# Performance work log

Hardware: AMD Instinct MI355X
Metric: run time of the kernel (lower is better)

## Reference

```python
import jax, jax.numpy as jnp
import numpy as np

B, T, D = 2, 1024, 2048      # batch, seq, model dim
E, F, K = 64, 512, 4          # n_experts, expert hidden, top-k
S, HS = 2, 512 * 4            # shared experts, shared hidden = expert_dim * topk


def setup_inputs() -> dict:
    key = jax.random.key(0)
    ks = jax.random.split(key, 9)
    s = 0.02
    f32 = jnp.float32
    return {
        "x": jax.random.normal(ks[0], (B, T, D), f32),
        "router_w": jax.random.normal(ks[1], (D, E), f32) * s,
        "router_bias": jnp.zeros((E,), f32),
        "wg": jax.random.normal(ks[2], (E, D, F), f32) * s,
        "wu": jax.random.normal(ks[3], (E, D, F), f32) * s,
        "wd": jax.random.normal(ks[4], (E, F, D), f32) * s,
        "swg": jax.random.normal(ks[5], (S, D, HS), f32) * s,
        "swu": jax.random.normal(ks[6], (S, D, HS), f32) * s,
        "swd": jax.random.normal(ks[7], (S, HS, D), f32) * s,
    }


def reference(x, router_w, router_bias, wg, wu, wd, swg, swu, swd):
    b, t, d = x.shape
    flat = x.reshape(b * t, d)                      # [N, D]
    n = flat.shape[0]

    # Router: softmax scores, top-k selection on (logits + bias)
    logits = flat @ router_w                         # [N, E]
    scores = jax.nn.softmax(logits, axis=-1)
    _, topk_idx = jax.lax.top_k(logits + router_bias, K)          # [N, K]
    topk_scores = jnp.take_along_axis(scores, topk_idx, axis=-1)  # [N, K]
    topk_scores = topk_scores / topk_scores.sum(axis=-1, keepdims=True)

    # Dense combine weights: w[n, e] = normalized score if expert e selected else 0
    comb = jnp.zeros((n, E), dtype=flat.dtype).at[
        jnp.arange(n)[:, None], topk_idx].set(topk_scores)        # [N, E]

    # Routed experts (SwiGLU), computed densely and masked by combine weights
    g = jax.nn.silu(jnp.einsum('nd,edf->nef', flat, wg))          # [N, E, F]
    u = jnp.einsum('nd,edf->nef', flat, wu)                       # [N, E, F]
    routed = jnp.einsum('ne,nef,efd->nd', comb, g * u, wd)        # [N, D]

    # Shared experts (always active, summed)
    sg = jax.nn.silu(jnp.einsum('nd,sdh->nsh', flat, swg))        # [N, S, HS]
    su = jnp.einsum('nd,sdh->nsh', flat, swu)
    shared = jnp.einsum('nsh,shd->nd', sg * su, swd)              # [N, D]

    return (routed + shared).reshape(b, t, d)
```

## Files before the change

### kernel.cpp

```cpp
#include <hip/hip_runtime.h>
#include <hip/hip_bf16.h>

typedef __bf16 bf16x8 __attribute__((ext_vector_type(8)));
typedef float f32x4 __attribute__((ext_vector_type(4)));
typedef unsigned short u16x4 __attribute__((ext_vector_type(4)));
typedef unsigned short u16x8 __attribute__((ext_vector_type(8)));

#define DEVI __device__ __forceinline__

constexpr int N_TOK = 2048;
constexpr int DIM   = 2048;
constexpr int NEXP  = 64;
constexpr int FDIM  = 512;
constexpr int TOPK  = 4;
constexpr int NSH   = 2;
constexpr int HSH   = 2048;

#define WAIT_VM0 asm volatile("s_waitcnt vmcnt(0)" ::: "memory")
#define WAIT_VM3 asm volatile("s_waitcnt vmcnt(3)" ::: "memory")
#define WAIT_VM4 asm volatile("s_waitcnt vmcnt(4)" ::: "memory")
#define WAIT_VM6 asm volatile("s_waitcnt vmcnt(6)" ::: "memory")
#define WAIT_LG0 asm volatile("s_waitcnt lgkmcnt(0)" ::: "memory")
#define SBAR __builtin_amdgcn_s_barrier()

DEVI unsigned short f2b(float f) {
  union { float fv; unsigned u; } v; v.fv = f;
  unsigned r = v.u + 0x7fffu + ((v.u >> 16) & 1u);
  return (unsigned short)(r >> 16);
}
DEVI float b2f(unsigned short h) {
  union { unsigned u; float f; } v; v.u = ((unsigned)h) << 16;
  return v.f;
}
DEVI void gll16(const void* g, void* l) {
  __builtin_amdgcn_global_load_lds((const __attribute__((address_space(1))) unsigned*)g,
                                   (__attribute__((address_space(3))) unsigned*)l, 16, 0, 0);
}
DEVI unsigned cvtpk(float lo, float hi) {
  unsigned r;
  asm("v_cvt_pk_bf16_f32 %0, %1, %2" : "=v"(r) : "v"(lo), "v"(hi));
  return r;
}
DEVI bf16x8 fragB(const float* base, int str) {
  union { unsigned u[4]; bf16x8 v; } r;
  #pragma unroll
  for (int p = 0; p < 4; ++p) r.u[p] = cvtpk(base[(2 * p) * str], base[(2 * p + 1) * str]);
  return r.v;
}

__global__ void cvt_x_kernel(const float* __restrict__ x, unsigned short* __restrict__ xb) {
  const size_t i = ((size_t)blockIdx.x * 256 + threadIdx.x) * 8;
  const float4 a = *reinterpret_cast<const float4*>(x + i);
  const float4 b = *reinterpret_cast<const float4*>(x + i + 4);
  u16x8 o;
  o[0] = f2b(a.x); o[1] = f2b(a.y); o[2] = f2b(a.z); o[3] = f2b(a.w);
  o[4] = f2b(b.x); o[5] = f2b(b.y); o[6] = f2b(b.z); o[7] = f2b(b.w);
  *reinterpret_cast<u16x8*>(xb + i) = o;
}

__global__ __launch_bounds__(256)
void tr_shared_kernel(const float* __restrict__ swu, const float* __restrict__ swg,
                      const float* __restrict__ swd, unsigned short* __restrict__ swuT,
                      unsigned short* __restrict__ swgT, unsigned short* __restrict__ swdT) {
  __shared__ float Lf[64][68];
  const int tid = threadIdx.x;
  const int r0 = blockIdx.x * 64, c0 = blockIdx.y * 64;
  const int z = blockIdx.z, mat = z >> 1;
  const size_t soff = (size_t)(z & 1) * DIM * HSH;
  const float* in = (mat == 0 ? swu : mat == 1 ? swg : swd) + soff;
  unsigned short* ot = (mat == 0 ? swuT : mat == 1 ? swgT : swdT) + soff;
  #pragma unroll
  for (int j = 0; j < 4; ++j) {
    const int idx = j * 1024 + tid * 4;
    const int row = idx >> 6, col = idx & 63;
    const float4 v = *reinterpret_cast<const float4*>(in + (size_t)(r0 + row) * 2048 + c0 + col);
    *reinterpret_cast<float4*>(&Lf[row][col]) = v;
  }
  __syncthreads();
  #pragma unroll
  for (int j = 0; j < 4; ++j) {
    const int idx = j * 1024 + tid * 4;
    const int orow = idx >> 6, ocol = idx & 63;
    u16x4 o;
    o[0] = f2b(Lf[ocol][orow]);     o[1] = f2b(Lf[ocol + 1][orow]);
    o[2] = f2b(Lf[ocol + 2][orow]); o[3] = f2b(Lf[ocol + 3][orow]);
    *reinterpret_cast<u16x4*>(ot + (size_t)(c0 + orow) * 2048 + r0 + ocol) = o;
  }
}

__global__ __launch_bounds__(256)
void router_kernel(const float* __restrict__ x, const float* __restrict__ rw,
                   const float* __restrict__ rb, int* __restrict__ cnt,
                   int* __restrict__ listTok, float* __restrict__ listW,
                   int* __restrict__ tokEP) {
  __shared__ float Lx[8][128];
  const int tid = threadIdx.x;
  const int lane = tid & 63;
  const int wave = tid >> 6;
  const int tokBase = blockIdx.x * 8;

  float acc0 = 0.f, acc1 = 0.f;
  for (int dc = 0; dc < DIM; dc += 128) {
    __syncthreads();
    {
      const int idx = tid * 4;
      const int row = idx >> 7, col = idx & 127;
      *reinterpret_cast<float4*>(&Lx[row][col]) =
          *reinterpret_cast<const float4*>(x + (size_t)(tokBase + row) * DIM + dc + col);
    }
    __syncthreads();
    #pragma unroll 16
    for (int dd = 0; dd < 128; ++dd) {
      const float r = rw[(size_t)(dc + dd) * NEXP + lane];
      acc0 = fmaf(Lx[wave * 2 + 0][dd], r, acc0);
      acc1 = fmaf(Lx[wave * 2 + 1][dd], r, acc1);
    }
  }

  const float bias = rb[lane];
  #pragma unroll
  for (int t = 0; t < 2; ++t) {
    const float v = (t == 0) ? acc0 : acc1;
    const int token = tokBase + wave * 2 + t;
    float m = v;
    #pragma unroll
    for (int o = 32; o > 0; o >>= 1) m = fmaxf(m, __shfl_xor(m, o));
    const float p = expf(v - m);
    float ss = p;
    #pragma unroll
    for (int o = 32; o > 0; o >>= 1) ss += __shfl_xor(ss, o);
    const float score = p / ss;
    float cur = v + bias;
    float wk[TOPK]; int ik[TOPK]; float wsum = 0.f;
    #pragma unroll
    for (int k = 0; k < TOPK; ++k) {
      float tm = cur;
      #pragma unroll
      for (int o = 32; o > 0; o >>= 1) tm = fmaxf(tm, __shfl_xor(tm, o));
      const unsigned long long msk = __ballot(cur == tm);
      const int sel = (int)__builtin_ctzll(msk);
      const float w = __shfl(score, sel);
      wk[k] = w; ik[k] = sel; wsum += w;
      if (lane == sel) cur = -3.4e38f;
    }
    if (lane < TOPK) {
      const int e = ik[lane];
      const float w = wk[lane] / wsum;
      const int slot = atomicAdd(&cnt[e], 1);
      listTok[(size_t)e * N_TOK + slot] = token;
      listW[(size_t)e * N_TOK + slot] = w;
      tokEP[token * TOPK + lane] = (e << 16) | slot;
    }
  }
}

__global__ void scan_kernel(const int* __restrict__ cnt, int* __restrict__ off) {
  if (threadIdx.x == 0) {
    int s = 0;
    for (int e = 0; e < NEXP; ++e) { off[e] = s; s += cnt[e]; }
  }
}

__global__ __launch_bounds__(256, 3)
void up_routed(const unsigned short* __restrict__ xb,
               const float* __restrict__ Wu, const float* __restrict__ Wg,
               const int* __restrict__ cnt, const int* __restrict__ off,
               const int* __restrict__ listTok, const float* __restrict__ listW,
               unsigned short* __restrict__ H) {
  constexpr int NT = DIM / 32;
  const int tid = threadIdx.x;
  const int f0 = blockIdx.x * 64;
  const int e  = blockIdx.y;
  const int m0 = blockIdx.z * 128;
  const int c = cnt[e];
  if (m0 >= c) return;
  const int rcnt = min(128, c - m0);
  const int rowbase = off[e] + m0;

  __shared__ __align__(16) unsigned short Al[2][4][128][8];
  __shared__ __align__(16) float Bf[2][2][32][64];
  __shared__ float wSs[128];

  if (tid < 128) wSs[tid] = (tid < rcnt) ? listW[(size_t)e * N_TOK + m0 + tid] : 0.f;
  WAIT_LG0;

  const int wid = tid >> 6, l = tid & 63;
  const int wm = wid >> 1, wn = wid & 1;
  const int lc = l & 15, hi = l >> 4;

  const int t0 = listTok[(size_t)e * N_TOK + m0 + min(l, rcnt - 1)];
  const int t1 = listTok[(size_t)e * N_TOK + m0 + min(64 + l, rcnt - 1)];
  const unsigned short* pa0 = xb + (size_t)t0 * DIM;
  const unsigned short* pa1 = xb + (size_t)t1 * DIM;
  const unsigned short* pas = (wid & 1) ? pa1 : pa0;
  const float* pbu = Wu + (size_t)e * DIM * FDIM + (size_t)(l >> 4) * FDIM + f0 + (l & 15) * 4;
  const float* pbg = Wg + (size_t)e * DIM * FDIM + (size_t)(l >> 4) * FDIM + f0 + (l & 15) * 4;

  auto stage = [&](int g, int b) {
    const int d0 = g * 32;
    gll16(pas + d0 + (wid >> 1) * 8,      &Al[b][wid >> 1][(wid & 1) * 64][0]);
    gll16(pas + d0 + (wid >> 1) * 8 + 16, &Al[b][(wid >> 1) + 2][(wid & 1) * 64][0]);
    gll16(pbu + (size_t)(d0 + 4 * wid) * FDIM,      &Bf[b][0][4 * wid][0]);
    gll16(pbu + (size_t)(d0 + 4 * wid + 16) * FDIM, &Bf[b][0][4 * wid + 16][0]);
    gll16(pbg + (size_t)(d0 + 4 * wid) * FDIM,      &Bf[b][1][4 * wid][0]);
    gll16(pbg + (size_t)(d0 + 4 * wid + 16) * FDIM, &Bf[b][1][4 * wid + 16][0]);
  };

  f32x4 aU[4][2], aG[4][2];
  #pragma unroll
  for (int i = 0; i < 4; ++i)
    #pragma unroll
    for (int j = 0; j < 2; ++j) { aU[i][j] = f32x4{0,0,0,0}; aG[i][j] = f32x4{0,0,0,0}; }

  stage(0, 0);
  for (int g = 0; g < NT; ++g) {
    const int b = g & 1;
    if (g + 1 < NT) { stage(g + 1, b ^ 1); WAIT_VM6; } else { WAIT_VM0; }
    SBAR;
    bf16x8 af[4];
    #pragma unroll
    for (int mi = 0; mi < 4; ++mi)
      af[mi] = *reinterpret_cast<const bf16x8*>(&Al[b][hi][wm * 64 + mi * 16 + lc][0]);
    #pragma unroll
    for (int ni = 0; ni < 2; ++ni) {
      const bf16x8 bu = fragB(&Bf[b][0][hi * 8][wn * 32 + ni * 16 + lc], 64);
      const bf16x8 bg = fragB(&Bf[b][1][hi * 8][wn * 32 + ni * 16 + lc], 64);
      #pragma unroll
      for (int mi = 0; mi < 4; ++mi) {
        aU[mi][ni] = __builtin_amdgcn_mfma_f32_16x16x32_bf16(af[mi], bu, aU[mi][ni], 0, 0, 0);
        aG[mi][ni] = __builtin_amdgcn_mfma_f32_16x16x32_bf16(af[mi], bg, aG[mi][ni], 0, 0, 0);
      }
    }
    SBAR;
  }

  #pragma unroll
  for (int mi = 0; mi < 4; ++mi)
    #pragma unroll
    for (int ni = 0; ni < 2; ++ni)
      #pragma unroll
      for (int r2 = 0; r2 < 4; ++r2) {
        const int row = wm * 64 + mi * 16 + hi * 4 + r2;
        if (row < rcnt) {
          const int col = f0 + wn * 32 + ni * 16 + lc;
          const float g = aG[mi][ni][r2], u = aU[mi][ni][r2];
          const float h = (g / (1.f + __expf(-g))) * u * wSs[row];
          H[(size_t)(rowbase + row) * FDIM + col] = f2b(h);
        }
      }
}

__global__ __launch_bounds__(256, 3)
void down_routed(const unsigned short* __restrict__ Hr, const float* __restrict__ wd,
                 const int* __restrict__ cnt, const int* __restrict__ off,
                 unsigned short* __restrict__ P) {
  constexpr int NT = FDIM / 32;
  const int tid = threadIdx.x;
  const int x0 = blockIdx.x * 128;
  const int e  = blockIdx.y;
  const int m0 = blockIdx.z * 128;
  const int c = cnt[e];
  if (m0 >= c) return;
  const int rcnt = min(128, c - m0);
  const int rowbase = off[e] + m0;

  __shared__ __align__(16) unsigned short Al[2][4][128][8];
  __shared__ __align__(16) float Bf[2][32][128];

  const int wid = tid >> 6, l = tid & 63;
  const int wm = wid >> 1, wn = wid & 1;
  const int lc = l & 15, hi = l >> 4;

  const unsigned short* pa0 = Hr + (size_t)(rowbase + min(l, rcnt - 1)) * FDIM;
  const unsigned short* pa1 = Hr + (size_t)(rowbase + min(64 + l, rcnt - 1)) * FDIM;
  const unsigned short* pas = (wid & 1) ? pa1 : pa0;
  const float* pB = wd + (size_t)e * FDIM * DIM + (size_t)(l >> 5) * DIM + x0 + (l & 31) * 4;

  auto stage = [&](int g, int b) {
    const int d0 = g * 32;
    gll16(pas + d0 + (wid >> 1) * 8,      &Al[b][wid >> 1][(wid & 1) * 64][0]);
    gll16(pas + d0 + (wid >> 1) * 8 + 16, &Al[b][(wid >> 1) + 2][(wid & 1) * 64][0]);
    #pragma unroll
    for (int cc = 0; cc < 4; ++cc) {
      const int i = cc * 4 + wid;
      gll16(pB + (size_t)(d0 + 2 * i) * DIM, &Bf[b][2 * i][0]);
    }
  };

  f32x4 acc[4][4];
  #pragma unroll
  for (int i = 0; i < 4; ++i)
    #pragma unroll
    for (int j = 0; j < 4; ++j) acc[i][j] = f32x4{0,0,0,0};

  stage(0, 0);
  for (int g = 0; g < NT; ++g) {
    const int b = g & 1;
    if (g + 1 < NT) { stage(g + 1, b ^ 1); WAIT_VM6; } else { WAIT_VM0; }
    SBAR;
    bf16x8 af[4];
    #pragma unroll
    for (int mi = 0; mi < 4; ++mi)
      af[mi] = *reinterpret_cast<const bf16x8*>(&Al[b][hi][wm * 64 + mi * 16 + lc][0]);
    #pragma unroll
    for (int ni = 0; ni < 4; ++ni) {
      const bf16x8 bq = fragB(&Bf[b][hi * 8][wn * 64 + ni * 16 + lc], 128);
      #pragma unroll
      for (int mi = 0; mi < 4; ++mi)
        acc[mi][ni] = __builtin_amdgcn_mfma_f32_16x16x32_bf16(af[mi], bq, acc[mi][ni], 0, 0, 0);
    }
    SBAR;
  }

  #pragma unroll
  for (int mi = 0; mi < 4; ++mi)
    #pragma unroll
    for (int ni = 0; ni < 4; ++ni)
      #pragma unroll
      for (int r2 = 0; r2 < 4; ++r2) {
        const int row = wm * 64 + mi * 16 + hi * 4 + r2;
        if (row < rcnt) {
          const int col = x0 + wn * 64 + ni * 16 + lc;
          P[(size_t)(rowbase + row) * DIM + col] = f2b(acc[mi][ni][r2]);
        }
      }
}

__global__ __launch_bounds__(256, 4)
void up_shared(const unsigned short* __restrict__ xb,
               const unsigned short* __restrict__ WuT, const unsigned short* __restrict__ WgT,
               unsigned short* __restrict__ H) {
  constexpr int NT = DIM / 32;
  const int tid = threadIdx.x;
  const int f0 = blockIdx.x * 64;
  const int s  = blockIdx.y;
  const int m0 = blockIdx.z * 128;

  __shared__ __align__(16) unsigned short Al[2][4][128][8];
  __shared__ __align__(16) unsigned short Bu[2][4][64][8];
  __shared__ __align__(16) unsigned short Bg[2][4][64][8];

  const int wid = tid >> 6, l = tid & 63;
  const int wm = wid >> 1, wn = wid & 1;
  const int lc = l & 15, hi = l >> 4;

  const unsigned short* pa0 = xb + (size_t)(m0 + l) * DIM;
  const unsigned short* pa1 = xb + (size_t)(m0 + 64 + l) * DIM;
  const unsigned short* pas = (wid & 1) ? pa1 : pa0;
  const unsigned short* pbu = WuT + (size_t)s * HSH * DIM + (size_t)(f0 + l) * DIM;
  const unsigned short* pbg = WgT + (size_t)s * HSH * DIM + (size_t)(f0 + l) * DIM;

  auto stage = [&](int g, int b) {
    const int d0 = g * 32;
    gll16(pas + d0 + (wid >> 1) * 8,      &Al[b][wid >> 1][(wid & 1) * 64][0]);
    gll16(pas + d0 + (wid >> 1) * 8 + 16, &Al[b][(wid >> 1) + 2][(wid & 1) * 64][0]);
    gll16(pbu + d0 + wid * 8, &Bu[b][wid][0][0]);
    gll16(pbg + d0 + wid * 8, &Bg[b][wid][0][0]);
  };

  f32x4 aU[4][2], aG[4][2];
  #pragma unroll
  for (int i = 0; i < 4; ++i)
    #pragma unroll
    for (int j = 0; j < 2; ++j) { aU[i][j] = f32x4{0,0,0,0}; aG[i][j] = f32x4{0,0,0,0}; }

  stage(0, 0);
  for (int g = 0; g < NT; ++g) {
    const int b = g & 1;
    if (g + 1 < NT) { stage(g + 1, b ^ 1); WAIT_VM4; } else { WAIT_VM0; }
    SBAR;
    bf16x8 af[4], bu[2], bg[2];
    #pragma unroll
    for (int mi = 0; mi < 4; ++mi)
      af[mi] = *reinterpret_cast<const bf16x8*>(&Al[b][hi][wm * 64 + mi * 16 + lc][0]);
    #pragma unroll
    for (int ni = 0; ni < 2; ++ni) {
      bu[ni] = *reinterpret_cast<const bf16x8*>(&Bu[b][hi][wn * 32 + ni * 16 + lc][0]);
      bg[ni] = *reinterpret_cast<const bf16x8*>(&Bg[b][hi][wn * 32 + ni * 16 + lc][0]);
    }
    #pragma unroll
    for (int mi = 0; mi < 4; ++mi)
      #pragma unroll
      for (int ni = 0; ni < 2; ++ni) {
        aU[mi][ni] = __builtin_amdgcn_mfma_f32_16x16x32_bf16(af[mi], bu[ni], aU[mi][ni], 0, 0, 0);
        aG[mi][ni] = __builtin_amdgcn_mfma_f32_16x16x32_bf16(af[mi], bg[ni], aG[mi][ni], 0, 0, 0);
      }
    SBAR;
  }

  #pragma unroll
  for (int mi = 0; mi < 4; ++mi)
    #pragma unroll
    for (int ni = 0; ni < 2; ++ni)
      #pragma unroll
      for (int r2 = 0; r2 < 4; ++r2) {
        const int row = wm * 64 + mi * 16 + hi * 4 + r2;
        const int col = f0 + wn * 32 + ni * 16 + lc;
        const float g = aG[mi][ni][r2], u = aU[mi][ni][r2];
        H[((size_t)s * N_TOK + m0 + row) * HSH + col] = f2b((g / (1.f + __expf(-g))) * u);
      }
}

__global__ __launch_bounds__(256, 4)
void down_shared(const unsigned short* __restrict__ Hs, const unsigned short* __restrict__ swdT,
                 float* __restrict__ out) {
  constexpr int NT = 2 * HSH / 32;
  const int tid = threadIdx.x;
  const int x0 = blockIdx.x * 128;
  const int m0 = blockIdx.z * 64;

  __shared__ __align__(16) unsigned short Al[2][4][64][8];
  __shared__ __align__(16) unsigned short Bl[2][4][128][8];

  const int wid = tid >> 6, l = tid & 63;
  const int wm = wid >> 1, wn = wid & 1;
  const int lc = l & 15, hi = l >> 4;

  const unsigned short* paA = Hs + (size_t)(m0 + l) * HSH;
  const unsigned short* pb0 = swdT + (size_t)(x0 + l) * HSH;
  const unsigned short* pb1 = swdT + (size_t)(x0 + 64 + l) * HSH;
  const unsigned short* pbs = (wid & 1) ? pb1 : pb0;

  auto stage = [&](int g, int b) {
    const int seg = g >> 6;
    const int dk = (g & 63) * 32;
    const size_t aoff = (size_t)seg * N_TOK * HSH;
    const size_t boff = (size_t)seg * HSH * DIM;
    gll16(paA + aoff + dk + wid * 8, &Al[b][wid][0][0]);
    gll16(pbs + boff + dk + (wid >> 1) * 8,      &Bl[b][wid >> 1][(wid & 1) * 64][0]);
    gll16(pbs + boff + dk + (wid >> 1) * 8 + 16, &Bl[b][(wid >> 1) + 2][(wid & 1) * 64][0]);
  };

  f32x4 acc[2][4];
  #pragma unroll
  for (int i = 0; i < 2; ++i)
    #pragma unroll
    for (int j = 0; j < 4; ++j) acc[i][j] = f32x4{0,0,0,0};

  stage(0, 0);
  for (int g = 0; g < NT; ++g) {
    const int b = g & 1;
    if (g + 1 < NT) { stage(g + 1, b ^ 1); WAIT_VM3; } else { WAIT_VM0; }
    SBAR;
    bf16x8 af[2], bq[4];
    #pragma unroll
    for (int mi = 0; mi < 2; ++mi)
      af[mi] = *reinterpret_cast<const bf16x8*>(&Al[b][hi][wm * 32 + mi * 16 + lc][0]);
    #pragma unroll
    for (int ni = 0; ni < 4; ++ni)
      bq[ni] = *reinterpret_cast<const bf16x8*>(&Bl[b][hi][wn * 64 + ni * 16 + lc][0]);
    #pragma unroll
    for (int mi = 0; mi < 2; ++mi)
      #pragma unroll
      for (int ni = 0; ni < 4; ++ni)
        acc[mi][ni] = __builtin_amdgcn_mfma_f32_16x16x32_bf16(af[mi], bq[ni], acc[mi][ni], 0, 0, 0);
    SBAR;
  }

  #pragma unroll
  for (int mi = 0; mi < 2; ++mi)
    #pragma unroll
    for (int ni = 0; ni < 4; ++ni)
      #pragma unroll
      for (int r2 = 0; r2 < 4; ++r2) {
        const int row = wm * 32 + mi * 16 + hi * 4 + r2;
        const int col = x0 + wn * 64 + ni * 16 + lc;
        out[(size_t)(m0 + row) * DIM + col] = acc[mi][ni][r2];
      }
}

__global__ __launch_bounds__(256)
void combine_kernel(const int* __restrict__ tokEP, const int* __restrict__ off,
                    const unsigned short* __restrict__ P, float* __restrict__ out) {
  const int n = blockIdx.x;
  const int tid = threadIdx.x;
  int rows[4];
  #pragma unroll
  for (int k = 0; k < TOPK; ++k) {
    const int ep = tokEP[n * TOPK + k];
    rows[k] = off[ep >> 16] + (ep & 0xffff);
  }
  const int cc = tid * 8;
  float* po = out + (size_t)n * DIM + cc;
  float4 o0 = *reinterpret_cast<const float4*>(po);
  float4 o1 = *reinterpret_cast<const float4*>(po + 4);
  #pragma unroll
  for (int k = 0; k < TOPK; ++k) {
    const u16x8 v = *reinterpret_cast<const u16x8*>(P + (size_t)rows[k] * DIM + cc);
    o0.x += b2f(v[0]); o0.y += b2f(v[1]); o0.z += b2f(v[2]); o0.w += b2f(v[3]);
    o1.x += b2f(v[4]); o1.y += b2f(v[5]); o1.z += b2f(v[6]); o1.w += b2f(v[7]);
  }
  *reinterpret_cast<float4*>(po) = o0;
  *reinterpret_cast<float4*>(po + 4) = o1;
}

extern "C" void kernel_launch(void* const* d_in, const int* in_sizes, int n_in,
                              void* d_out, int out_size, void* d_ws, size_t ws_size,
                              hipStream_t stream) {
  const float* x   = (const float*)d_in[0];
  const float* rw  = (const float*)d_in[1];
  const float* rb  = (const float*)d_in[2];
  const float* wg  = (const float*)d_in[3];
  const float* wu  = (const float*)d_in[4];
  const float* wd  = (const float*)d_in[5];
  const float* swg = (const float*)d_in[6];
  const float* swu = (const float*)d_in[7];
  const float* swd = (const float*)d_in[8];
  float* out = (float*)d_out;
  char* ws = (char*)d_ws;

  int* cnt = (int*)ws;
  int* off = (int*)(ws + 256);
  int* tokEP = (int*)(ws + 4096);
  int* listTok = (int*)(ws + 64 * 1024);
  float* listW = (float*)(ws + 576 * 1024);
  unsigned short* xb   = (unsigned short*)(ws + (size_t) 2 * 1024 * 1024);
  unsigned short* Hr   = (unsigned short*)(ws + (size_t)10 * 1024 * 1024);
  unsigned short* Hs   = (unsigned short*)(ws + (size_t)18 * 1024 * 1024);
  unsigned short* swuT = (unsigned short*)(ws + (size_t)34 * 1024 * 1024);
  unsigned short* swgT = (unsigned short*)(ws + (size_t)50 * 1024 * 1024);
  unsigned short* swdT = (unsigned short*)(ws + (size_t)66 * 1024 * 1024);
  unsigned short* P    = (unsigned short*)(ws + (size_t)82 * 1024 * 1024);

  hipMemsetAsync(cnt, 0, NEXP * sizeof(int), stream);
  cvt_x_kernel<<<(N_TOK * DIM) / (256 * 8), 256, 0, stream>>>(x, xb);
  tr_shared_kernel<<<dim3(32, 32, 6), 256, 0, stream>>>(swu, swg, swd, swuT, swgT, swdT);
  router_kernel<<<N_TOK / 8, 256, 0, stream>>>(x, rw, rb, cnt, listTok, listW, tokEP);
  scan_kernel<<<1, 64, 0, stream>>>(cnt, off);

  up_routed<<<dim3(FDIM / 64, NEXP, 16), 256, 0, stream>>>(
      xb, wu, wg, cnt, off, listTok, listW, Hr);
  up_shared<<<dim3(HSH / 64, NSH, N_TOK / 128), 256, 0, stream>>>(
      xb, swuT, swgT, Hs);
  down_shared<<<dim3(DIM / 128, 1, N_TOK / 64), 256, 0, stream>>>(
      Hs, swdT, out);
  down_routed<<<dim3(DIM / 128, NEXP, 16), 256, 0, stream>>>(
      Hr, wd, cnt, off, P);
  combine_kernel<<<N_TOK, 256, 0, stream>>>(tokEP, off, P, out);
}
```

Baseline: 717.4 us.

## Merge routed and shared GEMMs into two interleaved launches with single-buffered K=64 tiles

Merges up_routed and up_shared into one phase1 launch and down_routed and down_shared into one phase2 launch. Blocks are interleaved by a modulo mapping so shared-expert tiles run alongside routed-expert tiles, which is meant to fill the GPU better when many routed blocks exit early. It also swaps the double-buffered K=32 pipeline with explicit vmcnt waits for a single-buffered K=64 loop that uses __syncthreads, so loads no longer overlap compute. Merging into one kernel may also raise register and LDS pressure for the lighter branch.

```diff
diff --git a/kernel.cpp b/kernel.cpp
--- a/kernel.cpp
+++ b/kernel.cpp
@@ -15,13 +15,6 @@
 constexpr int TOPK  = 4;
 constexpr int NSH   = 2;
 constexpr int HSH   = 2048;
-
-#define WAIT_VM0 asm volatile("s_waitcnt vmcnt(0)" ::: "memory")
-#define WAIT_VM3 asm volatile("s_waitcnt vmcnt(3)" ::: "memory")
-#define WAIT_VM4 asm volatile("s_waitcnt vmcnt(4)" ::: "memory")
-#define WAIT_VM6 asm volatile("s_waitcnt vmcnt(6)" ::: "memory")
-#define WAIT_LG0 asm volatile("s_waitcnt lgkmcnt(0)" ::: "memory")
-#define SBAR __builtin_amdgcn_s_barrier()
 
 DEVI unsigned short f2b(float f) {
   union { float fv; unsigned u; } v; v.fv = f;
@@ -162,311 +155,299 @@
 }
 
 __global__ __launch_bounds__(256, 3)
-void up_routed(const unsigned short* __restrict__ xb,
-               const float* __restrict__ Wu, const float* __restrict__ Wg,
-               const int* __restrict__ cnt, const int* __restrict__ off,
-               const int* __restrict__ listTok, const float* __restrict__ listW,
-               unsigned short* __restrict__ H) {
-  constexpr int NT = DIM / 32;
+void phase1(const unsigned short* __restrict__ xb,
+            const float* __restrict__ Wu, const float* __restrict__ Wg,
+            const unsigned short* __restrict__ WuT, const unsigned short* __restrict__ WgT,
+            const int* __restrict__ cnt, const int* __restrict__ off,
+            const int* __restrict__ listTok, const float* __restrict__ listW,
+            unsigned short* __restrict__ Hr, unsigned short* __restrict__ Hs) {
+  __shared__ __align__(16) char smem[49152];
+  __shared__ float wSs[128];
+
+  const int bid = blockIdx.x;
+  const int q = bid / 9, r9 = bid % 9;
   const int tid = threadIdx.x;
-  const int f0 = blockIdx.x * 64;
-  const int e  = blockIdx.y;
-  const int m0 = blockIdx.z * 128;
-  const int c = cnt[e];
-  if (m0 >= c) return;
-  const int rcnt = min(128, c - m0);
-  const int rowbase = off[e] + m0;
-
-  __shared__ __align__(16) unsigned short Al[2][4][128][8];
-  __shared__ __align__(16) float Bf[2][2][32][64];
-  __shared__ float wSs[128];
-
-  if (tid < 128) wSs[tid] = (tid < rcnt) ? listW[(size_t)e * N_TOK + m0 + tid] : 0.f;
-  WAIT_LG0;
-
   const int wid = tid >> 6, l = tid & 63;
   const int wm = wid >> 1, wn = wid & 1;
   const int lc = l & 15, hi = l >> 4;
 
-  const int t0 = listTok[(size_t)e * N_TOK + m0 + min(l, rcnt - 1)];
-  const int t1 = listTok[(size_t)e * N_TOK + m0 + min(64 + l, rcnt - 1)];
-  const unsigned short* pa0 = xb + (size_t)t0 * DIM;
-  const unsigned short* pa1 = xb + (size_t)t1 * DIM;
-  const unsigned short* pas = (wid & 1) ? pa1 : pa0;
-  const float* pbu = Wu + (size_t)e * DIM * FDIM + (size_t)(l >> 4) * FDIM + f0 + (l & 15) * 4;
-  const float* pbg = Wg + (size_t)e * DIM * FDIM + (size_t)(l >> 4) * FDIM + f0 + (l & 15) * 4;
-
-  auto stage = [&](int g, int b) {
-    const int d0 = g * 32;
-    gll16(pas + d0 + (wid >> 1) * 8,      &Al[b][wid >> 1][(wid & 1) * 64][0]);
-    gll16(pas + d0 + (wid >> 1) * 8 + 16, &Al[b][(wid >> 1) + 2][(wid & 1) * 64][0]);
-    gll16(pbu + (size_t)(d0 + 4 * wid) * FDIM,      &Bf[b][0][4 * wid][0]);
-    gll16(pbu + (size_t)(d0 + 4 * wid + 16) * FDIM, &Bf[b][0][4 * wid + 16][0]);
-    gll16(pbg + (size_t)(d0 + 4 * wid) * FDIM,      &Bf[b][1][4 * wid][0]);
-    gll16(pbg + (size_t)(d0 + 4 * wid + 16) * FDIM, &Bf[b][1][4 * wid + 16][0]);
-  };
-
-  f32x4 aU[4][2], aG[4][2];
-  #pragma unroll
-  for (int i = 0; i < 4; ++i)
-    #pragma unroll
-    for (int j = 0; j < 2; ++j) { aU[i][j] = f32x4{0,0,0,0}; aG[i][j] = f32x4{0,0,0,0}; }
-
-  stage(0, 0);
-  for (int g = 0; g < NT; ++g) {
-    const int b = g & 1;
-    if (g + 1 < NT) { stage(g + 1, b ^ 1); WAIT_VM6; } else { WAIT_VM0; }
-    SBAR;
-    bf16x8 af[4];
+  if (r9 == 8) {
+    const int f0 = (q & 31) * 64;
+    const int s  = (q >> 5) & 1;
+    const int m0 = (q >> 6) * 128;
+    auto Al = reinterpret_cast<unsigned short (*)[128][8]>(smem);
+    auto Bu = reinterpret_cast<unsigned short (*)[64][8]>(smem + 16384);
+    auto Bg = reinterpret_cast<unsigned short (*)[64][8]>(smem + 24576);
+
+    const unsigned short* pa0 = xb + (size_t)(m0 + l) * DIM;
+    const unsigned short* pa1 = xb + (size_t)(m0 + 64 + l) * DIM;
+    const unsigned short* pbu = WuT + (size_t)s * HSH * DIM + (size_t)(f0 + l) * DIM;
+    const unsigned short* pbg = WgT + (size_t)s * HSH * DIM + (size_t)(f0 + l) * DIM;
+
+    f32x4 aU[4][2], aG[4][2];
+    #pragma unroll
+    for (int i = 0; i < 4; ++i)
+      #pragma unroll
+      for (int j = 0; j < 2; ++j) { aU[i][j] = f32x4{0,0,0,0}; aG[i][j] = f32x4{0,0,0,0}; }
+
+    for (int g = 0; g < DIM / 64; ++g) {
+      const int d0 = g * 64;
+      gll16(pa0 + d0 + wid * 8,       &Al[wid][0][0]);
+      gll16(pa1 + d0 + wid * 8,       &Al[wid][64][0]);
+      gll16(pa0 + d0 + (wid + 4) * 8, &Al[wid + 4][0][0]);
+      gll16(pa1 + d0 + (wid + 4) * 8, &Al[wid + 4][64][0]);
+      gll16(pbu + d0 + wid * 8,       &Bu[wid][0][0]);
+      gll16(pbu + d0 + (wid + 4) * 8, &Bu[wid + 4][0][0]);
+      gll16(pbg + d0 + wid * 8,       &Bg[wid][0][0]);
+      gll16(pbg + d0 + (wid + 4) * 8, &Bg[wid + 4][0][0]);
+      __syncthreads();
+      #pragma unroll
+      for (int ks = 0; ks < 2; ++ks) {
+        bf16x8 af[4], bu[2], bg[2];
+        #pragma unroll
+        for (int mi = 0; mi < 4; ++mi)
+          af[mi] = *reinterpret_cast<const bf16x8*>(&Al[ks * 4 + hi][wm * 64 + mi * 16 + lc][0]);
+        #pragma unroll
+        for (int ni = 0; ni < 2; ++ni) {
+          bu[ni] = *reinterpret_cast<const bf16x8*>(&Bu[ks * 4 + hi][wn * 32 + ni * 16 + lc][0]);
+          bg[ni] = *reinterpret_cast<const bf16x8*>(&Bg[ks * 4 + hi][wn * 32 + ni * 16 + lc][0]);
+        }
+        #pragma unroll
+        for (int mi = 0; mi < 4; ++mi)
+          #pragma unroll
+          for (int ni = 0; ni < 2; ++ni) {
+            aU[mi][ni] = __builtin_amdgcn_mfma_f32_16x16x32_bf16(af[mi], bu[ni], aU[mi][ni], 0, 0, 0);
+            aG[mi][ni] = __builtin_amdgcn_mfma_f32_16x16x32_bf16(af[mi], bg[ni], aG[mi][ni], 0, 0, 0);
+          }
+      }
+      __syncthreads();
+    }
+
     #pragma unroll
     for (int mi = 0; mi < 4; ++mi)
-      af[mi] = *reinterpret_cast<const bf16x8*>(&Al[b][hi][wm * 64 + mi * 16 + lc][0]);
-    #pragma unroll
-    for (int ni = 0; ni < 2; ++ni) {
-      const bf16x8 bu = fragB(&Bf[b][0][hi * 8][wn * 32 + ni * 16 + lc], 64);
-      const bf16x8 bg = fragB(&Bf[b][1][hi * 8][wn * 32 + ni * 16 + lc], 64);
-      #pragma unroll
-      for (int mi = 0; mi < 4; ++mi) {
-        aU[mi][ni] = __builtin_amdgcn_mfma_f32_16x16x32_bf16(af[mi], bu, aU[mi][ni], 0, 0, 0);
-        aG[mi][ni] = __builtin_amdgcn_mfma_f32_16x16x32_bf16(af[mi], bg, aG[mi][ni], 0, 0, 0);
-      }
-    }
-    SBAR;
-  }
-
-  #pragma unroll
-  for (int mi = 0; mi < 4; ++mi)
-    #pragma unroll
-    for (int ni = 0; ni < 2; ++ni)
-      #pragma unroll
-      for (int r2 = 0; r2 < 4; ++r2) {
-        const int row = wm * 64 + mi * 16 + hi * 4 + r2;
-        if (row < rcnt) {
+      #pragma unroll
+      for (int ni = 0; ni < 2; ++ni)
+        #pragma unroll
+        for (int r2 = 0; r2 < 4; ++r2) {
+          const int row = wm * 64 + mi * 16 + hi * 4 + r2;
           const int col = f0 + wn * 32 + ni * 16 + lc;
           const float g = aG[mi][ni][r2], u = aU[mi][ni][r2];
-          const float h = (g / (1.f + __expf(-g))) * u * wSs[row];
-          H[(size_t)(rowbase + row) * FDIM + col] = f2b(h);
-        }
+          Hs[((size_t)s * N_TOK + m0 + row) * HSH + col] = f2b((g / (1.f + __expf(-g))) * u);
+        }
+  } else {
+    const int idx = q * 8 + r9;
+    const int e  = idx >> 7;
+    const int f0 = ((idx >> 4) & 7) * 64;
+    const int m0 = (idx & 15) * 128;
+    const int c = cnt[e];
+    if (m0 >= c) return;
+    const int rcnt = min(128, c - m0);
+    const int rowbase = off[e] + m0;
+
+    auto Al  = reinterpret_cast<unsigned short (*)[128][8]>(smem);
+    auto Bfu = reinterpret_cast<float (*)[64]>(smem + 16384);
+    auto Bfg = reinterpret_cast<float (*)[64]>(smem + 32768);
+
+    if (tid < 128) wSs[tid] = (tid < rcnt) ? listW[(size_t)e * N_TOK + m0 + tid] : 0.f;
+
+    const int t0 = listTok[(size_t)e * N_TOK + m0 + min(l, rcnt - 1)];
+    const int t1 = listTok[(size_t)e * N_TOK + m0 + min(64 + l, rcnt - 1)];
+    const unsigned short* pa0 = xb + (size_t)t0 * DIM;
+    const unsigned short* pa1 = xb + (size_t)t1 * DIM;
+    const float* pbu = Wu + (size_t)e * DIM * FDIM + (size_t)(l >> 4) * FDIM + f0 + (l & 15) * 4;
+    const float* pbg = Wg + (size_t)e * DIM * FDIM + (size_t)(l >> 4) * FDIM + f0 + (l & 15) * 4;
+
+    f32x4 aU[4][2], aG[4][2];
+    #pragma unroll
+    for (int i = 0; i < 4; ++i)
+      #pragma unroll
+      for (int j = 0; j < 2; ++j) { aU[i][j] = f32x4{0,0,0,0}; aG[i][j] = f32x4{0,0,0,0}; }
+
+    for (int g = 0; g < DIM / 64; ++g) {
+      const int d0 = g * 64;
+      gll16(pa0 + d0 + wid * 8,       &Al[wid][0][0]);
+      gll16(pa1 + d0 + wid * 8,       &Al[wid][64][0]);
+      gll16(pa0 + d0 + (wid + 4) * 8, &Al[wid + 4][0][0]);
+      gll16(pa1 + d0 + (wid + 4) * 8, &Al[wid + 4][64][0]);
+      #pragma unroll
+      for (int j = 0; j < 4; ++j) {
+        const int rr = wid * 16 + j * 4;
+        gll16(pbu + (size_t)(d0 + rr) * FDIM, &Bfu[rr][0]);
+        gll16(pbg + (size_t)(d0 + rr) * FDIM, &Bfg[rr][0]);
       }
+      __syncthreads();
+      #pragma unroll
+      for (int ks = 0; ks < 2; ++ks) {
+        bf16x8 af[4];
+        #pragma unroll
+        for (int mi = 0; mi < 4; ++mi)
+          af[mi] = *reinterpret_cast<const bf16x8*>(&Al[ks * 4 + hi][wm * 64 + mi * 16 + lc][0]);
+        #pragma unroll
+        for (int ni = 0; ni < 2; ++ni) {
+          const bf16x8 bu = fragB(&Bfu[ks * 32 + hi * 8][wn * 32 + ni * 16 + lc], 64);
+          const bf16x8 bg = fragB(&Bfg[ks * 32 + hi * 8][wn * 32 + ni * 16 + lc], 64);
+          #pragma unroll
+          for (int mi = 0; mi < 4; ++mi) {
+            aU[mi][ni] = __builtin_amdgcn_mfma_f32_16x16x32_bf16(af[mi], bu, aU[mi][ni], 0, 0, 0);
+            aG[mi][ni] = __builtin_amdgcn_mfma_f32_16x16x32_bf16(af[mi], bg, aG[mi][ni], 0, 0, 0);
+          }
+        }
+      }
+      __syncthreads();
+    }
+
+    #pragma unroll
+    for (int mi = 0; mi < 4; ++mi)
+      #pragma unroll
+      for (int ni = 0; ni < 2; ++ni)
+        #pragma unroll
+        for (int r2 = 0; r2 < 4; ++r2) {
+          const int row = wm * 64 + mi * 16 + hi * 4 + r2;
+          if (row < rcnt) {
+            const int col = f0 + wn * 32 + ni * 16 + lc;
+            const float g = aG[mi][ni][r2], u = aU[mi][ni][r2];
+            const float h = (g / (1.f + __expf(-g))) * u * wSs[row];
+            Hr[(size_t)(rowbase + row) * FDIM + col] = f2b(h);
+          }
+        }
+  }
 }
 
 __global__ __launch_bounds__(256, 3)
-void down_routed(const unsigned short* __restrict__ Hr, const float* __restrict__ wd,
-                 const int* __restrict__ cnt, const int* __restrict__ off,
-                 unsigned short* __restrict__ P) {
-  constexpr int NT = FDIM / 32;
+void phase2(const unsigned short* __restrict__ Hr, const unsigned short* __restrict__ Hs,
+            const float* __restrict__ wd, const unsigned short* __restrict__ swdT,
+            const int* __restrict__ cnt, const int* __restrict__ off,
+            unsigned short* __restrict__ P, float* __restrict__ out) {
+  __shared__ __align__(16) char smem[49152];
+
+  const int bid = blockIdx.x;
+  const int q = bid / 33, r33 = bid % 33;
   const int tid = threadIdx.x;
-  const int x0 = blockIdx.x * 128;
-  const int e  = blockIdx.y;
-  const int m0 = blockIdx.z * 128;
-  const int c = cnt[e];
-  if (m0 >= c) return;
-  const int rcnt = min(128, c - m0);
-  const int rowbase = off[e] + m0;
-
-  __shared__ __align__(16) unsigned short Al[2][4][128][8];
-  __shared__ __align__(16) float Bf[2][32][128];
-
   const int wid = tid >> 6, l = tid & 63;
   const int wm = wid >> 1, wn = wid & 1;
   const int lc = l & 15, hi = l >> 4;
 
-  const unsigned short* pa0 = Hr + (size_t)(rowbase + min(l, rcnt - 1)) * FDIM;
-  const unsigned short* pa1 = Hr + (size_t)(rowbase + min(64 + l, rcnt - 1)) * FDIM;
-  const unsigned short* pas = (wid & 1) ? pa1 : pa0;
-  const float* pB = wd + (size_t)e * FDIM * DIM + (size_t)(l >> 5) * DIM + x0 + (l & 31) * 4;
-
-  auto stage = [&](int g, int b) {
-    const int d0 = g * 32;
-    gll16(pas + d0 + (wid >> 1) * 8,      &Al[b][wid >> 1][(wid & 1) * 64][0]);
-    gll16(pas + d0 + (wid >> 1) * 8 + 16, &Al[b][(wid >> 1) + 2][(wid & 1) * 64][0]);
-    #pragma unroll
-    for (int cc = 0; cc < 4; ++cc) {
-      const int i = cc * 4 + wid;
-      gll16(pB + (size_t)(d0 + 2 * i) * DIM, &Bf[b][2 * i][0]);
-    }
-  };
-
-  f32x4 acc[4][4];
-  #pragma unroll
-  for (int i = 0; i < 4; ++i)
-    #pragma unroll
-    for (int j = 0; j < 4; ++j) acc[i][j] = f32x4{0,0,0,0};
-
-  stage(0, 0);
-  for (int g = 0; g < NT; ++g) {
-    const int b = g & 1;
-    if (g + 1 < NT) { stage(g + 1, b ^ 1); WAIT_VM6; } else { WAIT_VM0; }
-    SBAR;
-    bf16x8 af[4];
+  if (r33 == 32) {
+    const int x0 = (q & 15) * 128;
+    const int m0 = (q >> 4) * 64;
+    auto Al = reinterpret_cast<unsigned short (*)[64][8]>(smem);
+    auto Bl = reinterpret_cast<unsigned short (*)[128][8]>(smem + 8192);
+
+    const unsigned short* paA = Hs + (size_t)(m0 + l) * HSH;
+    const unsigned short* pb0 = swdT + (size_t)(x0 + l) * HSH;
+    const unsigned short* pb1 = swdT + (size_t)(x0 + 64 + l) * HSH;
+
+    f32x4 acc[2][4];
+    #pragma unroll
+    for (int i = 0; i < 2; ++i)
+      #pragma unroll
+      for (int j = 0; j < 4; ++j) acc[i][j] = f32x4{0,0,0,0};
+
+    for (int g = 0; g < 2 * HSH / 64; ++g) {
+      const int seg = g >> 5;
+      const int dk = (g & 31) * 64;
+      const size_t aoff = (size_t)seg * N_TOK * HSH;
+      const size_t boff = (size_t)seg * HSH * DIM;
+      gll16(paA + aoff + dk + wid * 8,       &Al[wid][0][0]);
+      gll16(paA + aoff + dk + (wid + 4) * 8, &Al[wid + 4][0][0]);
+      gll16(pb0 + boff + dk + wid * 8,       &Bl[wid][0][0]);
+      gll16(pb1 + boff + dk + wid * 8,       &Bl[wid][64][0]);
+      gll16(pb0 + boff + dk + (wid + 4) * 8, &Bl[wid + 4][0][0]);
+      gll16(pb1 + boff + dk + (wid + 4) * 8, &Bl[wid + 4][64][0]);
+      __syncthreads();
+      #pragma unroll
+      for (int ks = 0; ks < 2; ++ks) {
+        bf16x8 af[2], bq[4];
+        #pragma unroll
+        for (int mi = 0; mi < 2; ++mi)
+          af[mi] = *reinterpret_cast<const bf16x8*>(&Al[ks * 4 + hi][wm * 32 + mi * 16 + lc][0]);
+        #pragma unroll
+        for (int ni = 0; ni < 4; ++ni)
+          bq[ni] = *reinterpret_cast<const bf16x8*>(&Bl[ks * 4 + hi][wn * 64 + ni * 16 + lc][0]);
+        #pragma unroll
+        for (int mi = 0; mi < 2; ++mi)
+          #pragma unroll
+          for (int ni = 0; ni < 4; ++ni)
+            acc[mi][ni] = __builtin_amdgcn_mfma_f32_16x16x32_bf16(af[mi], bq[ni], acc[mi][ni], 0, 0, 0);
+      }
+      __syncthreads();
+    }
+
+    #pragma unroll
+    for (int mi = 0; mi < 2; ++mi)
+      #pragma unroll
+      for (int ni = 0; ni < 4; ++ni)
+        #pragma unroll
+        for (int r2 = 0; r2 < 4; ++r2) {
+          const int row = wm * 32 + mi * 16 + hi * 4 + r2;
+          const int col = x0 + wn * 64 + ni * 16 + lc;
+          out[(size_t)(m0 + row) * DIM + col] = acc[mi][ni][r2];
+        }
+  } else {
+    const int idx = q * 32 + r33;
+    const int e  = idx >> 8;
+    const int x0 = ((idx >> 4) & 15) * 128;
+    const int m0 = (idx & 15) * 128;
+    const int c = cnt[e];
+    if (m0 >= c) return;
+    const int rcnt = min(128, c - m0);
+    const int rowbase = off[e] + m0;
+
+    auto Al = reinterpret_cast<unsigned short (*)[128][8]>(smem);
+    auto Bf = reinterpret_cast<float (*)[128]>(smem + 16384);
+
+    const unsigned short* pa0 = Hr + (size_t)(rowbase + min(l, rcnt - 1)) * FDIM;
+    const unsigned short* pa1 = Hr + (size_t)(rowbase + min(64 + l, rcnt - 1)) * FDIM;
+    const float* pB = wd + (size_t)e * FDIM * DIM + (size_t)(l >> 5) * DIM + x0 + (l & 31) * 4;
+
+    f32x4 acc[4][4];
+    #pragma unroll
+    for (int i = 0; i < 4; ++i)
+      #pragma unroll
+      for (int j = 0; j < 4; ++j) acc[i][j] = f32x4{0,0,0,0};
+
+    for (int g = 0; g < FDIM / 64; ++g) {
+      const int d0 = g * 64;
+      gll16(pa0 + d0 + wid * 8,       &Al[wid][0][0]);
+      gll16(pa1 + d0 + wid * 8,       &Al[wid][64][0]);
+      gll16(pa0 + d0 + (wid + 4) * 8, &Al[wid + 4][0][0]);
+      gll16(pa1 + d0 + (wid + 4) * 8, &Al[wid + 4][64][0]);
+      #pragma unroll
+      for (int j = 0; j < 8; ++j) {
+        const int rr = wid * 16 + j * 2;
+        gll16(pB + (size_t)(d0 + rr) * DIM, &Bf[rr][0]);
+      }
+      __syncthreads();
+      #pragma unroll
+      for (int ks = 0; ks < 2; ++ks) {
+        bf16x8 af[4];
+        #pragma unroll
+        for (int mi = 0; mi < 4; ++mi)
+          af[mi] = *reinterpret_cast<const bf16x8*>(&Al[ks * 4 + hi][wm * 64 + mi * 16 + lc][0]);
+        #pragma unroll
+        for (int ni = 0; ni < 4; ++ni) {
+          const bf16x8 bq = fragB(&Bf[ks * 32 + hi * 8][wn * 64 + ni * 16 + lc], 128);
+          #pragma unroll
+          for (int mi = 0; mi < 4; ++mi)
+            acc[mi][ni] = __builtin_amdgcn_mfma_f32_16x16x32_bf16(af[mi], bq, acc[mi][ni], 0, 0, 0);
+        }
+      }
+      __syncthreads();
+    }
+
     #pragma unroll
     for (int mi = 0; mi < 4; ++mi)
-      af[mi] = *reinterpret_cast<const bf16x8*>(&Al[b][hi][wm * 64 + mi * 16 + lc][0]);
-    #pragma unroll
-    for (int ni = 0; ni < 4; ++ni) {
-      const bf16x8 bq = fragB(&Bf[b][hi * 8][wn * 64 + ni * 16 + lc], 128);
-      #pragma unroll
-      for (int mi = 0; mi < 4; ++mi)
-        acc[mi][ni] = __builtin_amdgcn_mfma_f32_16x16x32_bf16(af[mi], bq, acc[mi][ni], 0, 0, 0);
-    }
-    SBAR;
-  }
-
-  #pragma unroll
-  for (int mi = 0; mi < 4; ++mi)
-    #pragma unroll
-    for (int ni = 0; ni < 4; ++ni)
-      #pragma unroll
-      for (int r2 = 0; r2 < 4; ++r2) {
-        const int row = wm * 64 + mi * 16 + hi * 4 + r2;
-        if (row < rcnt) {
-          const int col = x0 + wn * 64 + ni * 16 + lc;
-          P[(size_t)(rowbase + row) * DIM + col] = f2b(acc[mi][ni][r2]);
-        }
-      }
-}
-
-__global__ __launch_bounds__(256, 4)
-void up_shared(const unsigned short* __restrict__ xb,
-               const unsigned short* __restrict__ WuT, const unsigned short* __restrict__ WgT,
-               unsigned short* __restrict__ H) {
-  constexpr int NT = DIM / 32;
-  const int tid = threadIdx.x;
-  const int f0 = blockIdx.x * 64;
-  const int s  = blockIdx.y;
-  const int m0 = blockIdx.z * 128;
-
-  __shared__ __align__(16) unsigned short Al[2][4][128][8];
-  __shared__ __align__(16) unsigned short Bu[2][4][64][8];
-  __shared__ __align__(16) unsigned short Bg[2][4][64][8];
-
-  const int wid = tid >> 6, l = tid & 63;
-  const int wm = wid >> 1, wn = wid & 1;
-  const int lc = l & 15, hi = l >> 4;
-
-  const unsigned short* pa0 = xb + (size_t)(m0 + l) * DIM;
-  const unsigned short* pa1 = xb + (size_t)(m0 + 64 + l) * DIM;
-  const unsigned short* pas = (wid & 1) ? pa1 : pa0;
-  const unsigned short* pbu = WuT + (size_t)s * HSH * DIM + (size_t)(f0 + l) * DIM;
-  const unsigned short* pbg = WgT + (size_t)s * HSH * DIM + (size_t)(f0 + l) * DIM;
-
-  auto stage = [&](int g, int b) {
-    const int d0 = g * 32;
-    gll16(pas + d0 + (wid >> 1) * 8,      &Al[b][wid >> 1][(wid & 1) * 64][0]);
-    gll16(pas + d0 + (wid >> 1) * 8 + 16, &Al[b][(wid >> 1) + 2][(wid & 1) * 64][0]);
-    gll16(pbu + d0 + wid * 8, &Bu[b][wid][0][0]);
-    gll16(pbg + d0 + wid * 8, &Bg[b][wid][0][0]);
-  };
-
-  f32x4 aU[4][2], aG[4][2];
-  #pragma unroll
-  for (int i = 0; i < 4; ++i)
-    #pragma unroll
-    for (int j = 0; j < 2; ++j) { aU[i][j] = f32x4{0,0,0,0}; aG[i][j] = f32x4{0,0,0,0}; }
-
-  stage(0, 0);
-  for (int g = 0; g < NT; ++g) {
-    const int b = g & 1;
-    if (g + 1 < NT) { stage(g + 1, b ^ 1); WAIT_VM4; } else { WAIT_VM0; }
-    SBAR;
-    bf16x8 af[4], bu[2], bg[2];
-    #pragma unroll
-    for (int mi = 0; mi < 4; ++mi)
-      af[mi] = *reinterpret_cast<const bf16x8*>(&Al[b][hi][wm * 64 + mi * 16 + lc][0]);
-    #pragma unroll
-    for (int ni = 0; ni < 2; ++ni) {
-      bu[ni] = *reinterpret_cast<const bf16x8*>(&Bu[b][hi][wn * 32 + ni * 16 + lc][0]);
-      bg[ni] = *reinterpret_cast<const bf16x8*>(&Bg[b][hi][wn * 32 + ni * 16 + lc][0]);
-    }
-    #pragma unroll
-    for (int mi = 0; mi < 4; ++mi)
-      #pragma unroll
-      for (int ni = 0; ni < 2; ++ni) {
-        aU[mi][ni] = __builtin_amdgcn_mfma_f32_16x16x32_bf16(af[mi], bu[ni], aU[mi][ni], 0, 0, 0);
-        aG[mi][ni] = __builtin_amdgcn_mfma_f32_16x16x32_bf16(af[mi], bg[ni], aG[mi][ni], 0, 0, 0);
-      }
-    SBAR;
-  }
-
-  #pragma unroll
-  for (int mi = 0; mi < 4; ++mi)
-    #pragma unroll
-    for (int ni = 0; ni < 2; ++ni)
-      #pragma unroll
-      for (int r2 = 0; r2 < 4; ++r2) {
-        const int row = wm * 64 + mi * 16 + hi * 4 + r2;
-        const int col = f0 + wn * 32 + ni * 16 + lc;
-        const float g = aG[mi][ni][r2], u = aU[mi][ni][r2];
-        H[((size_t)s * N_TOK + m0 + row) * HSH + col] = f2b((g / (1.f + __expf(-g))) * u);
-      }
-}
-
-__global__ __launch_bounds__(256, 4)
-void down_shared(const unsigned short* __restrict__ Hs, const unsigned short* __restrict__ swdT,
-                 float* __restrict__ out) {
-  constexpr int NT = 2 * HSH / 32;
-  const int tid = threadIdx.x;
-  const int x0 = blockIdx.x * 128;
-  const int m0 = blockIdx.z * 64;
-
-  __shared__ __align__(16) unsigned short Al[2][4][64][8];
-  __shared__ __align__(16) unsigned short Bl[2][4][128][8];
-
-  const int wid = tid >> 6, l = tid & 63;
-  const int wm = wid >> 1, wn = wid & 1;
-  const int lc = l & 15, hi = l >> 4;
-
-  const unsigned short* paA = Hs + (size_t)(m0 + l) * HSH;
-  const unsigned short* pb0 = swdT + (size_t)(x0 + l) * HSH;
-  const unsigned short* pb1 = swdT + (size_t)(x0 + 64 + l) * HSH;
-  const unsigned short* pbs = (wid & 1) ? pb1 : pb0;
-
-  auto stage = [&](int g, int b) {
-    const int seg = g >> 6;
-    const int dk = (g & 63) * 32;
-    const size_t aoff = (size_t)seg * N_TOK * HSH;
-    const size_t boff = (size_t)seg * HSH * DIM;
-    gll16(paA + aoff + dk + wid * 8, &Al[b][wid][0][0]);
-    gll16(pbs + boff + dk + (wid >> 1) * 8,      &Bl[b][wid >> 1][(wid & 1) * 64][0]);
-    gll16(pbs + boff + dk + (wid >> 1) * 8 + 16, &Bl[b][(wid >> 1) + 2][(wid & 1) * 64][0]);
-  };
-
-  f32x4 acc[2][4];
-  #pragma unroll
-  for (int i = 0; i < 2; ++i)
-    #pragma unroll
-    for (int j = 0; j < 4; ++j) acc[i][j] = f32x4{0,0,0,0};
-
-  stage(0, 0);
-  for (int g = 0; g < NT; ++g) {
-    const int b = g & 1;
-    if (g + 1 < NT) { stage(g + 1, b ^ 1); WAIT_VM3; } else { WAIT_VM0; }
-    SBAR;
-    bf16x8 af[2], bq[4];
-    #pragma unroll
-    for (int mi = 0; mi < 2; ++mi)
-      af[mi] = *reinterpret_cast<const bf16x8*>(&Al[b][hi][wm * 32 + mi * 16 + lc][0]);
-    #pragma unroll
-    for (int ni = 0; ni < 4; ++ni)
-      bq[ni] = *reinterpret_cast<const bf16x8*>(&Bl[b][hi][wn * 64 + ni * 16 + lc][0]);
-    #pragma unroll
-    for (int mi = 0; mi < 2; ++mi)
       #pragma unroll
       for (int ni = 0; ni < 4; ++ni)
-        acc[mi][ni] = __builtin_amdgcn_mfma_f32_16x16x32_bf16(af[mi], bq[ni], acc[mi][ni], 0, 0, 0);
-    SBAR;
-  }
-
-  #pragma unroll
-  for (int mi = 0; mi < 2; ++mi)
-    #pragma unroll
-    for (int ni = 0; ni < 4; ++ni)
-      #pragma unroll
-      for (int r2 = 0; r2 < 4; ++r2) {
-        const int row = wm * 32 + mi * 16 + hi * 4 + r2;
-        const int col = x0 + wn * 64 + ni * 16 + lc;
-        out[(size_t)(m0 + row) * DIM + col] = acc[mi][ni][r2];
-      }
+        #pragma unroll
+        for (int r2 = 0; r2 < 4; ++r2) {
+          const int row = wm * 64 + mi * 16 + hi * 4 + r2;
+          if (row < rcnt) {
+            const int col = x0 + wn * 64 + ni * 16 + lc;
+            P[(size_t)(rowbase + row) * DIM + col] = f2b(acc[mi][ni][r2]);
+          }
+        }
+  }
 }
 
 __global__ __launch_bounds__(256)
@@ -528,13 +509,7 @@
   router_kernel<<<N_TOK / 8, 256, 0, stream>>>(x, rw, rb, cnt, listTok, listW, tokEP);
   scan_kernel<<<1, 64, 0, stream>>>(cnt, off);
 
-  up_routed<<<dim3(FDIM / 64, NEXP, 16), 256, 0, stream>>>(
-      xb, wu, wg, cnt, off, listTok, listW, Hr);
-  up_shared<<<dim3(HSH / 64, NSH, N_TOK / 128), 256, 0, stream>>>(
-      xb, swuT, swgT, Hs);
-  down_shared<<<dim3(DIM / 128, 1, N_TOK / 64), 256, 0, stream>>>(
-      Hs, swdT, out);
-  down_routed<<<dim3(DIM / 128, NEXP, 16), 256, 0, stream>>>(
-      Hr, wd, cnt, off, P);
+  phase1<<<9216, 256, 0, stream>>>(xb, wu, wg, swuT, swgT, cnt, off, listTok, listW, Hr, Hs);
+  phase2<<<16896, 256, 0, stream>>>(Hr, Hs, wd, swdT, cnt, off, P, out);
   combine_kernel<<<N_TOK, 256, 0, stream>>>(tokEP, off, P, out);
 }
```

Result: slower. 734.5 us (+2.4%).
